# Performance work log

Measured on AMD Instinct MI355X. Metric: run time of the kernel, lower is better.

## Reference

```python
import jax, jax.numpy as jnp
import numpy as np

HIDDEN = 1024
NUM_TOTAL = 8
NUM_SHARED = 2
NUM_ROUTED = NUM_TOTAL - NUM_SHARED
TOP_K = 2
TOKENS = 16384
SCALE = 0.02


def setup_inputs() -> dict:
    key = jax.random.key(0)
    ks = jax.random.split(key, 12)
    h = HIDDEN
    inp = {
        "x": jax.random.normal(ks[0], (TOKENS, h), dtype=jnp.float32),
        # shared experts: [E_s, in, hidden] / [E_s, hidden] etc. (y = x @ W + b)
        "shared_w1": jax.random.normal(ks[1], (NUM_SHARED, h, h), jnp.float32) * SCALE,
        "shared_b1": jnp.zeros((NUM_SHARED, h), jnp.float32),
        "shared_w2": jax.random.normal(ks[2], (NUM_SHARED, h, h), jnp.float32) * SCALE,
        "shared_b2": jnp.zeros((NUM_SHARED, h), jnp.float32),
        # routed experts
        "routed_w1": jax.random.normal(ks[3], (NUM_ROUTED, h, h), jnp.float32) * SCALE,
        "routed_b1": jnp.zeros((NUM_ROUTED, h), jnp.float32),
        "routed_w2": jax.random.normal(ks[4], (NUM_ROUTED, h, h), jnp.float32) * SCALE,
        "routed_b2": jnp.zeros((NUM_ROUTED, h), jnp.float32),
        # router: Linear(hidden, num_routed)
        "router_w": jax.random.normal(ks[5], (h, NUM_ROUTED), jnp.float32) * SCALE,
        "router_b": jnp.zeros((NUM_ROUTED,), jnp.float32),
    }
    return inp


def _expert_all(x, w1, b1, w2, b2):
    # x: [B, H]; w1/w2: [E, H, H]; returns [B, E, H]
    hmid = jnp.tanh(jnp.einsum("bi,eio->beo", x, w1) + b1)
    return jnp.einsum("beh,eho->beo", hmid, w2) + b2


def reference(x, shared_w1, shared_b1, shared_w2, shared_b2,
              routed_w1, routed_b1, routed_w2, routed_b2,
              router_w, router_b):
    # shared experts: every token through every shared expert, summed
    shared_out = _expert_all(x, shared_w1, shared_b1, shared_w2, shared_b2).sum(axis=1)  # [B,H]

    # router softmax + top-k mask (original weights each expert by
    # routing_weights[:, i] * mask[:, i], i.e. NOT renormalized)
    logits = x @ router_w + router_b                       # [B, E_r]
    routing_weights = jax.nn.softmax(logits, axis=-1)      # [B, E_r]
    _, top_idx = jax.lax.top_k(routing_weights, TOP_K)     # [B, k]
    mask = jax.nn.one_hot(top_idx, NUM_ROUTED, dtype=routing_weights.dtype).sum(axis=1)  # [B, E_r]
    weight = routing_weights * mask                        # [B, E_r]

    # dense all-expert compute masked by top-k (faithful to source loop)
    expert_out = _expert_all(x, routed_w1, routed_b1, routed_w2, routed_b2)  # [B, E_r, H]
    routed_out = jnp.einsum("be,beh->bh", weight, expert_out)

    return shared_out + routed_out
```

## Files before the change

kernel.cpp:

```cpp
#include <hip/hip_runtime.h>
#include <hip/hip_bf16.h>

#define H 1024
#define B_TOK 16384
#define RTILES 262
#define RCAP   (RTILES * 128)

typedef __attribute__((ext_vector_type(8))) short s16x8;
typedef __attribute__((ext_vector_type(4))) float f32x4;

__device__ __forceinline__ short f2bf(float f) {
  __hip_bfloat16 h = __float2bfloat16(f);
  return __builtin_bit_cast(short, h);
}
__device__ __forceinline__ float bf2f(short s) {
  __hip_bfloat16 h = __builtin_bit_cast(__hip_bfloat16, s);
  return __bfloat162float(h);
}

__device__ __forceinline__ float fast_tanh(float x) {
  const float e = __expf(2.f * x);
  return 1.f - __fdividef(2.f, e + 1.f);
}

__device__ __forceinline__ void load_lds16(const short* g, short* l) {
  __builtin_amdgcn_global_load_lds((const __attribute__((address_space(1))) void*)g,
                                   (__attribute__((address_space(3))) void*)l,
                                   16, 0, 0);
}

__global__ void cvt_x_k(const float* __restrict__ x, short* __restrict__ xb) {
  const size_t i = ((size_t)blockIdx.x * blockDim.x + threadIdx.x) * 8;
  const float4 a = *(const float4*)(x + i);
  const float4 b = *(const float4*)(x + i + 4);
  s16x8 v;
  v[0] = f2bf(a.x); v[1] = f2bf(a.y); v[2] = f2bf(a.z); v[3] = f2bf(a.w);
  v[4] = f2bf(b.x); v[5] = f2bf(b.y); v[6] = f2bf(b.z); v[7] = f2bf(b.w);
  *(s16x8*)(xb + i) = v;
}

__global__ void transpose_k(const float* __restrict__ sw1, const float* __restrict__ rw1,
                            const float* __restrict__ sw2, const float* __restrict__ rw2,
                            short* __restrict__ w1t, short* __restrict__ w2t_sh,
                            short* __restrict__ w2t_r) {
  __shared__ float tile[64][65];
  const int z = blockIdx.z;
  const float* src;
  short* dst;
  int ldd = H, koff = 0;
  if (z < 8) {
    src = (z < 2) ? sw1 + (size_t)z * H * H : rw1 + (size_t)(z - 2) * H * H;
    dst = w1t + (size_t)z * H * H;
  } else if (z < 10) {
    const int e = z - 8;
    src = sw2 + (size_t)e * H * H;
    dst = w2t_sh; ldd = 2048; koff = e * 1024;
  } else {
    const int e = z - 10;
    src = rw2 + (size_t)e * H * H;
    dst = w2t_r + (size_t)e * H * H;
  }
  const int k0 = blockIdx.y * 64, n0 = blockIdx.x * 64;
  const int t = threadIdx.x;
#pragma unroll
  for (int i = 0; i < 4; ++i) {
    const int kk = (t >> 4) + 16 * i;
    const int nn = (t & 15) * 4;
    const float4 v = *(const float4*)(src + (size_t)(k0 + kk) * H + n0 + nn);
    tile[nn + 0][kk] = v.x; tile[nn + 1][kk] = v.y;
    tile[nn + 2][kk] = v.z; tile[nn + 3][kk] = v.w;
  }
  __syncthreads();
  const int nn = t >> 2;
  const int kk = (t & 3) * 16;
  s16x8 o0, o1;
#pragma unroll
  for (int u = 0; u < 8; ++u) {
    o0[u] = f2bf(tile[nn][kk + u]);
    o1[u] = f2bf(tile[nn][kk + 8 + u]);
  }
  short* drow = dst + (size_t)(n0 + nn) * ldd + koff + k0 + kk;
  *(s16x8*)(drow) = o0;
  *(s16x8*)(drow + 8) = o1;
}

__global__ void logits_k(const float* __restrict__ x, const float* __restrict__ rw,
                         const float* __restrict__ rb, int2* __restrict__ tk) {
  const int lane = threadIdx.x & 63;
  const int b = blockIdx.x * 4 + (threadIdx.x >> 6);
  const float* xr = x + (size_t)b * H;
  float p[6] = {0.f, 0.f, 0.f, 0.f, 0.f, 0.f};
  for (int k = lane; k < H; k += 64) {
    const float xv = xr[k];
    const float* r = rw + k * 6;
#pragma unroll
    for (int e = 0; e < 6; ++e) p[e] += xv * r[e];
  }
#pragma unroll
  for (int e = 0; e < 6; ++e) {
    float v = p[e];
    for (int off = 32; off > 0; off >>= 1) v += __shfl_down(v, off);
    p[e] = v;
  }
  if (lane == 0) {
    float lg[6];
    float mx = -1e30f;
#pragma unroll
    for (int e = 0; e < 6; ++e) { lg[e] = p[e] + rb[e]; mx = fmaxf(mx, lg[e]); }
    float s = 0.f;
#pragma unroll
    for (int e = 0; e < 6; ++e) { lg[e] = __expf(lg[e] - mx); s += lg[e]; }
    const float inv = 1.f / s;
#pragma unroll
    for (int e = 0; e < 6; ++e) lg[e] *= inv;
    int i1 = 0;
#pragma unroll
    for (int e = 1; e < 6; ++e) if (lg[e] > lg[i1]) i1 = e;
    int i2 = (i1 == 0) ? 1 : 0;
#pragma unroll
    for (int e = 0; e < 6; ++e) if (e != i1 && lg[e] > lg[i2]) i2 = e;
    int2 v;
    v.x = i1 | ((int)(unsigned short)f2bf(lg[i1]) << 16);
    v.y = i2 | ((int)(unsigned short)f2bf(lg[i2]) << 16);
    tk[b] = v;
  }
}

__global__ void hist_k(const int2* __restrict__ tk, int* __restrict__ g) {
  __shared__ int h[6];
  const int t = threadIdx.x;
  if (t < 6) h[t] = 0;
  __syncthreads();
  const int2 v = tk[blockIdx.x * 256 + t];
  atomicAdd(&h[v.x & 0xffff], 1);
  atomicAdd(&h[v.y & 0xffff], 1);
  __syncthreads();
  if (t < 6) atomicAdd(&g[t], h[t]);
}

__global__ void prefix_k(int* __restrict__ g) {
  if (threadIdx.x == 0) {
    int run = 0;
#pragma unroll
    for (int e = 0; e < 6; ++e) {
      g[8 + e] = run; g[16 + e] = run;
      run += (g[e] + 127) & ~127;
    }
    g[14] = run;
  }
}

__global__ void scatter_k(const int2* __restrict__ tk, int* __restrict__ g,
                          int* __restrict__ asg) {
  __shared__ int lcnt[6];
  __shared__ int lbase[6];
  const int t = threadIdx.x;
  if (t < 6) lcnt[t] = 0;
  __syncthreads();
  const int tok = blockIdx.x * 256 + t;
  const int2 v = tk[tok];
  const int e1 = v.x & 0xffff, e2 = v.y & 0xffff;
  const int p1 = atomicAdd(&lcnt[e1], 1);
  const int p2 = atomicAdd(&lcnt[e2], 1);
  __syncthreads();
  if (t < 6) lbase[t] = atomicAdd(&g[16 + t], lcnt[t]);
  __syncthreads();
  asg[lbase[e1] + p1] = tok | (v.x & 0xffff0000);
  asg[lbase[e2] + p2] = tok | (v.y & 0xffff0000);
}

__device__ __forceinline__ void gemm_core64(const short* __restrict__ A, int lda,
                                            const short* __restrict__ Bt, int ldb, int K,
                                            short* smem, int m0, int n0,
                                            const int* __restrict__ asg, int acap,
                                            f32x4 acc[4][4]) {
  const int tid = threadIdx.x, lane = tid & 63, w = tid >> 6;
  const int q8 = (lane >> 4) * 8, r16 = lane & 15;
  const int wr = w >> 1, wc = w & 1;

  const short* gp[4];
#pragma unroll
  for (int ii = 0; ii < 4; ++ii) {
    const int c2 = w * 4 + ii;
    if (c2 < 8) {
      int slot = m0 + c2 * 16 + r16;
      int gr;
      if (asg) {
        int tv = asg[slot] & 0xffff;
        gr = tv < B_TOK ? tv : B_TOK - 1;
      } else {
        gr = slot < acap ? slot : acap - 1;
      }
      gp[ii] = A + (size_t)gr * lda + q8;
    } else {
      gp[ii] = Bt + (size_t)(n0 + (c2 - 8) * 16 + r16) * ldb + q8;
    }
  }
  short* lw0 = smem + w * 4096;
  short* lw1 = smem + 16384 + w * 4096;

#pragma unroll
  for (int i = 0; i < 8; ++i)
    load_lds16(gp[i >> 1] + (i & 1) * 32, lw0 + i * 512);

  int cur = 0;
  for (int k0 = 0; k0 < K; k0 += 64) {
    __syncthreads();
    const short* lc = cur ? smem + 16384 : smem;
    short* lwn = cur ? lw0 : lw1;
    if (k0 + 64 < K) {
#pragma unroll
      for (int i = 0; i < 8; ++i)
        load_lds16(gp[i >> 1] + (k0 + 64) + (i & 1) * 32, lwn + i * 512);
    }
#pragma unroll
    for (int s = 0; s < 2; ++s) {
      s16x8 af[4], bfv[4];
#pragma unroll
      for (int i = 0; i < 4; ++i)
        af[i] = *(const s16x8*)(lc + ((wr * 4 + i) * 2 + s) * 512 + lane * 8);
#pragma unroll
      for (int j = 0; j < 4; ++j)
        bfv[j] = *(const s16x8*)(lc + (16 + (wc * 4 + j) * 2 + s) * 512 + lane * 8);
#pragma unroll
      for (int i = 0; i < 4; ++i)
#pragma unroll
        for (int j = 0; j < 4; ++j)
          acc[i][j] = __builtin_amdgcn_mfma_f32_16x16x32_bf16(af[i], bfv[j], acc[i][j], 0, 0, 0);
    }
    cur ^= 1;
  }
}

template <int ROUTED>
__global__ __launch_bounds__(256) void gemm1_k(const short* __restrict__ A, int lda,
                                               const short* __restrict__ W1, int ldb, int K,
                                               const float* __restrict__ b1,
                                               short* __restrict__ Out, int ldo,
                                               const int* __restrict__ asg,
                                               const int* __restrict__ g, int rowcap) {
  const int m0 = blockIdx.x * 128, n0 = blockIdx.y * 128;
  const short* Bt = W1;
  const float* bias = b1;
  if (ROUTED) {
    if (m0 >= g[14]) return;
    int e = 0;
#pragma unroll
    for (int j = 1; j < 6; ++j) if (m0 >= g[8 + j]) e = j;
    Bt = W1 + (size_t)e * H * H;
    bias = b1 + (size_t)e * H;
  }
  __shared__ __align__(16) short smem[32768];
  f32x4 acc[4][4];
#pragma unroll
  for (int i = 0; i < 4; ++i)
#pragma unroll
    for (int j = 0; j < 4; ++j) acc[i][j] = (f32x4){0.f, 0.f, 0.f, 0.f};
  gemm_core64(A, lda, Bt, ldb, K, smem, m0, n0, ROUTED ? asg : nullptr, 1 << 30, acc);

  const int tid = threadIdx.x, lane = tid & 63, w = tid >> 6;
  const int wr = w >> 1, wc = w & 1, q = lane >> 4, c16 = lane & 15;
  __syncthreads();
#pragma unroll
  for (int j = 0; j < 4; ++j) {
    const int colL = wc * 64 + j * 16 + c16;
    const float bv = bias[n0 + colL];
#pragma unroll
    for (int i = 0; i < 4; ++i)
#pragma unroll
      for (int r = 0; r < 4; ++r)
        smem[(wr * 64 + i * 16 + q * 4 + r) * 128 + colL] = f2bf(fast_tanh(acc[i][j][r] + bv));
  }
  __syncthreads();
#pragma unroll
  for (int p = 0; p < 8; ++p) {
    const int rowL = p * 16 + (tid >> 4);
    const int colL = (tid & 15) * 8;
    const int gr = m0 + rowL;
    if (gr < rowcap)
      *(s16x8*)(Out + (size_t)gr * ldo + n0 + colL) = *(const s16x8*)(smem + rowL * 128 + colL);
  }
}

template <int MODE>
__global__ __launch_bounds__(256) void gemm2_k(const short* __restrict__ A, int lda,
                                               const short* __restrict__ W2, int ldb, int K,
                                               const float* __restrict__ b2a,
                                               const float* __restrict__ b2b,
                                               float* __restrict__ Out,
                                               const int* __restrict__ asg,
                                               const int* __restrict__ g, int acap) {
  const int m0 = blockIdx.x * 128, n0 = blockIdx.y * 128;
  const short* Bt = W2;
  const float* bias = b2a;
  if (MODE == 3) {
    if (m0 >= g[14]) return;
    int e = 0;
#pragma unroll
    for (int j = 1; j < 6; ++j) if (m0 >= g[8 + j]) e = j;
    Bt = W2 + (size_t)e * H * H;
    bias = b2a + (size_t)e * H;
  }
  __shared__ __align__(16) short smem[32768];
  f32x4 acc[4][4];
#pragma unroll
  for (int i = 0; i < 4; ++i)
#pragma unroll
    for (int j = 0; j < 4; ++j) acc[i][j] = (f32x4){0.f, 0.f, 0.f, 0.f};
  gemm_core64(A, lda, Bt, ldb, K, smem, m0, n0, nullptr, acap, acc);

  const int tid = threadIdx.x, lane = tid & 63, w = tid >> 6;
  const int wr = w >> 1, wc = w & 1, q = lane >> 4, c16 = lane & 15;

  if (MODE == 0) {
    float* cs = (float*)smem;
    __syncthreads();
#pragma unroll
    for (int half = 0; half < 2; ++half) {
      if (wr == half) {
#pragma unroll
        for (int j = 0; j < 4; ++j) {
          const int colL = wc * 64 + j * 16 + c16;
          const float bv = b2a[n0 + colL] + b2b[n0 + colL];
#pragma unroll
          for (int i = 0; i < 4; ++i)
#pragma unroll
            for (int r = 0; r < 4; ++r)
              cs[(i * 16 + q * 4 + r) * 128 + colL] = acc[i][j][r] + bv;
        }
      }
      __syncthreads();
#pragma unroll
      for (int p = 0; p < 8; ++p) {
        const int rowL = p * 8 + (tid >> 5);
        const int colL = (tid & 31) * 4;
        *(float4*)(Out + (size_t)(m0 + half * 64 + rowL) * H + n0 + colL) =
            *(const float4*)(cs + rowL * 128 + colL);
      }
      __syncthreads();
    }
  } else {
    const int mb = m0 + wr * 64, nb = n0 + wc * 64;
#pragma unroll
    for (int i = 0; i < 4; ++i) {
      int av[4];
#pragma unroll
      for (int r = 0; r < 4; ++r) av[r] = asg[mb + i * 16 + q * 4 + r];
#pragma unroll
      for (int j = 0; j < 4; ++j) {
        const int col = nb + j * 16 + c16;
        const float bv = bias[col];
#pragma unroll
        for (int r = 0; r < 4; ++r) {
          if (av[r] == -1) continue;
          const int tok = av[r] & 0xffff;
          const float wt = bf2f((short)((unsigned)av[r] >> 16));
          atomicAdd(&Out[(size_t)tok * H + col], (acc[i][j][r] + bv) * wt);
        }
      }
    }
  }
}

extern "C" void kernel_launch(void* const* d_in, const int* in_sizes, int n_in,
                              void* d_out, int out_size, void* d_ws, size_t ws_size,
                              hipStream_t stream) {
  const float* x        = (const float*)d_in[0];
  const float* sw1      = (const float*)d_in[1];
  const float* sb1      = (const float*)d_in[2];
  const float* sw2      = (const float*)d_in[3];
  const float* sb2      = (const float*)d_in[4];
  const float* rw1      = (const float*)d_in[5];
  const float* rb1      = (const float*)d_in[6];
  const float* rw2      = (const float*)d_in[7];
  const float* rb2      = (const float*)d_in[8];
  const float* router_w = (const float*)d_in[9];
  const float* router_b = (const float*)d_in[10];
  float* out = (float*)d_out;

  char* ws = (char*)d_ws;
  short* xb     = (short*)(ws);
  short* w1t    = (short*)(ws + (size_t)33554432);
  short* w2t_r  = (short*)(ws + (size_t)50331648);
  short* w2t_sh = (short*)(ws + (size_t)62914560);
  short* hm_sh  = (short*)(ws + (size_t)67108864);
  short* hm_r   = (short*)(ws + (size_t)62914560);
  int2*  tk     = (int2*)hm_sh;
  int*   g      = (int*)(ws + (size_t)134217728);
  int*   asg    = (int*)(ws + (size_t)134217984);

  hipMemsetAsync(g, 0, 64, stream);
  hipMemsetAsync(asg, 0xFF, RCAP * sizeof(int), stream);

  cvt_x_k<<<8192, 256, 0, stream>>>(x, xb);
  transpose_k<<<dim3(16, 16, 16), 256, 0, stream>>>(sw1, rw1, sw2, rw2, w1t, w2t_sh, w2t_r);
  logits_k<<<4096, 256, 0, stream>>>(x, router_w, router_b, tk);
  hist_k<<<64, 256, 0, stream>>>(tk, g);
  prefix_k<<<1, 64, 0, stream>>>(g);
  scatter_k<<<64, 256, 0, stream>>>(tk, g, asg);

  gemm1_k<0><<<dim3(128, 16), 256, 0, stream>>>(xb, H, w1t, H, H, sb1, hm_sh, 2048,
                                                nullptr, nullptr, 1 << 30);
  gemm2_k<0><<<dim3(128, 8), 256, 0, stream>>>(hm_sh, 2048, w2t_sh, 2048, 2048,
                                               sb2, sb2 + H, out, nullptr, nullptr, 1 << 30);

  gemm1_k<1><<<dim3(RTILES, 8), 256, 0, stream>>>(xb, H, w1t + (size_t)2 * H * H, H, H,
                                                  rb1, hm_r, H, asg, g, RCAP);
  gemm2_k<3><<<dim3(RTILES, 8), 256, 0, stream>>>(hm_r, H, w2t_r, H, H,
                                                  rb2, nullptr, out, asg, g, RCAP);
}
```

Measured before the change: 837.9 us.

## Deepen GEMM K-loop prefetch to two stages with explicit waitcnt and setprio

Restructures the GEMM main loop so global-to-LDS loads run two K-steps ahead instead of one. Explicit vmcnt waits and raw s_barrier replace the generic __syncthreads. The next buffer is refilled only after all waves have read the current LDS fragments. s_setprio is raised around MFMA bursts to favour matrix issue across waves. This aims to hide more global memory latency and cut barrier overhead, at the risk of subtle synchronisation errors if the hand-written vmcnt counts do not match the issued loads.

```diff
diff --git a/kernel.cpp b/kernel.cpp
--- a/kernel.cpp
+++ b/kernel.cpp
@@ -202,32 +202,59 @@
 #pragma unroll
   for (int i = 0; i < 8; ++i)
     load_lds16(gp[i >> 1] + (i & 1) * 32, lw0 + i * 512);
-
+#pragma unroll
+  for (int i = 0; i < 8; ++i)
+    load_lds16(gp[i >> 1] + 64 + (i & 1) * 32, lw1 + i * 512);
+
+  const int nsteps = K >> 6;
   int cur = 0;
-  for (int k0 = 0; k0 < K; k0 += 64) {
-    __syncthreads();
+  for (int t = 0; t < nsteps; ++t) {
+    if (t + 1 < nsteps)
+      asm volatile("s_waitcnt vmcnt(8)" ::: "memory");
+    else
+      asm volatile("s_waitcnt vmcnt(0)" ::: "memory");
+    __builtin_amdgcn_sched_barrier(0);
+    __builtin_amdgcn_s_barrier();
     const short* lc = cur ? smem + 16384 : smem;
-    short* lwn = cur ? lw0 : lw1;
-    if (k0 + 64 < K) {
+    short* lwn = cur ? lw1 : lw0;
+
+    s16x8 af0[4], bf0[4], af1[4], bf1[4];
+#pragma unroll
+    for (int i = 0; i < 4; ++i)
+      af0[i] = *(const s16x8*)(lc + ((wr * 4 + i) * 2 + 0) * 512 + lane * 8);
+#pragma unroll
+    for (int j = 0; j < 4; ++j)
+      bf0[j] = *(const s16x8*)(lc + (16 + (wc * 4 + j) * 2 + 0) * 512 + lane * 8);
+    __builtin_amdgcn_s_setprio(1);
+#pragma unroll
+    for (int i = 0; i < 4; ++i)
+#pragma unroll
+      for (int j = 0; j < 4; ++j)
+        acc[i][j] = __builtin_amdgcn_mfma_f32_16x16x32_bf16(af0[i], bf0[j], acc[i][j], 0, 0, 0);
+    __builtin_amdgcn_s_setprio(0);
+
+#pragma unroll
+    for (int i = 0; i < 4; ++i)
+      af1[i] = *(const s16x8*)(lc + ((wr * 4 + i) * 2 + 1) * 512 + lane * 8);
+#pragma unroll
+    for (int j = 0; j < 4; ++j)
+      bf1[j] = *(const s16x8*)(lc + (16 + (wc * 4 + j) * 2 + 1) * 512 + lane * 8);
+    asm volatile("s_waitcnt lgkmcnt(0)" ::: "memory");
+    __builtin_amdgcn_sched_barrier(0);
+    __builtin_amdgcn_s_barrier();
+
+    if (t + 2 < nsteps) {
 #pragma unroll
       for (int i = 0; i < 8; ++i)
-        load_lds16(gp[i >> 1] + (k0 + 64) + (i & 1) * 32, lwn + i * 512);
+        load_lds16(gp[i >> 1] + (t + 2) * 64 + (i & 1) * 32, lwn + i * 512);
     }
-#pragma unroll
-    for (int s = 0; s < 2; ++s) {
-      s16x8 af[4], bfv[4];
-#pragma unroll
-      for (int i = 0; i < 4; ++i)
-        af[i] = *(const s16x8*)(lc + ((wr * 4 + i) * 2 + s) * 512 + lane * 8);
+    __builtin_amdgcn_s_setprio(1);
+#pragma unroll
+    for (int i = 0; i < 4; ++i)
 #pragma unroll
       for (int j = 0; j < 4; ++j)
-        bfv[j] = *(const s16x8*)(lc + (16 + (wc * 4 + j) * 2 + s) * 512 + lane * 8);
-#pragma unroll
-      for (int i = 0; i < 4; ++i)
-#pragma unroll
-        for (int j = 0; j < 4; ++j)
-          acc[i][j] = __builtin_amdgcn_mfma_f32_16x16x32_bf16(af[i], bfv[j], acc[i][j], 0, 0, 0);
-    }
+        acc[i][j] = __builtin_amdgcn_mfma_f32_16x16x32_bf16(af1[i], bf1[j], acc[i][j], 0, 0, 0);
+    __builtin_amdgcn_s_setprio(0);
     cur ^= 1;
   }
 }
```

Result: faster. 791.3 us (-5.6%).
